# Optimization experiments

Measured on AMD Instinct MI355X. Metric: run time of the kernel, lower is better.

## Reference

```python
import jax, jax.numpy as jnp
import numpy as np

NUM_GRAPHS = 1024


def setup_inputs() -> dict:
    key = jax.random.key(0)
    k1, k2, k3, k4 = jax.random.split(key, 4)
    N, IN, OUT = 500000, 128, 128
    x = jax.random.normal(k1, (N, IN), dtype=jnp.float32)
    batch_id = jnp.sort(jax.random.randint(k2, (N,), 0, NUM_GRAPHS))
    # torch Linear: weight [out_features, in_features_total]
    W = jax.random.normal(k3, (OUT, 2 * IN), dtype=jnp.float32) * (1.0 / np.sqrt(2 * IN))
    b = jax.random.normal(k4, (OUT,), dtype=jnp.float32) * 0.01
    return {"x": x, "batch_id": batch_id, "W": W, "b": b}


def reference(x, batch_id, W, b):
    # global_mean_pool: segment-mean of x over batch_id -> [G, IN]
    sums = jax.ops.segment_sum(x, batch_id, num_segments=NUM_GRAPHS)
    counts = jax.ops.segment_sum(jnp.ones((x.shape[0],), dtype=x.dtype), batch_id,
                                 num_segments=NUM_GRAPHS)
    mean = sums / jnp.maximum(counts, 1.0)[:, None]  # [G, IN]
    # gather per-graph context back to each node, concat, linear
    g_per_node = mean[batch_id]                      # [N, IN]
    inp = jnp.concatenate([x, g_per_node], axis=-1)  # [N, 2*IN]
    return inp @ W.T + b                             # [N, OUT]
```

## Files before the change

kernel.cpp:

```cpp
#include <hip/hip_runtime.h>
#include <hip/hip_bf16.h>


#define G_NUM 1024
#define IN_F 128
#define OUT_F 128

typedef __attribute__((ext_vector_type(8))) short short8;
typedef __attribute__((ext_vector_type(4))) float f32x4;

static __device__ __forceinline__ unsigned short f2bf(float f) {
    union { float f; unsigned u; } v; v.f = f;
    unsigned u = v.u;
    unsigned r = (u + 0x7FFFu + ((u >> 16) & 1u)) >> 16;
    return (unsigned short)r;
}

static __device__ __forceinline__ short8 pack8(float4 a, float4 b) {
    short8 o;
    o[0] = (short)f2bf(a.x); o[1] = (short)f2bf(a.y);
    o[2] = (short)f2bf(a.z); o[3] = (short)f2bf(a.w);
    o[4] = (short)f2bf(b.x); o[5] = (short)f2bf(b.y);
    o[6] = (short)f2bf(b.z); o[7] = (short)f2bf(b.w);
    return o;
}

__global__ void k_wcvt(const float* __restrict__ W, unsigned short* __restrict__ W1b) {
    int i = blockIdx.x * 256 + threadIdx.x;
    if (i < OUT_F * IN_F) {
        int o = i >> 7, k = i & 127;
        W1b[i] = f2bf(W[o * 256 + k]);
    }
}

__global__ __launch_bounds__(256) void k_mean_ctx(
        const float* __restrict__ x, const int* __restrict__ bid,
        const float* __restrict__ W, const float* __restrict__ b,
        float* __restrict__ ctx, int N) {
    int g = blockIdx.x;
    int tid = threadIdx.x;

    int lo = 0, hi = N;
    while (lo < hi) { int m = (lo + hi) >> 1; if (bid[m] < g) lo = m + 1; else hi = m; }
    int start = lo;
    int lo2 = start, hi2 = N;
    while (lo2 < hi2) { int m = (lo2 + hi2) >> 1; if (bid[m] < g + 1) lo2 = m + 1; else hi2 = m; }
    int end = lo2;
    int cnt = end - start;

    __shared__ float4 red[8][32];
    __shared__ float ms[IN_F];

    int c4 = tid & 31;
    int rg = tid >> 5;
    float4 s0 = make_float4(0.f, 0.f, 0.f, 0.f);
    float4 s1 = s0, s2 = s0, s3 = s0;

    int r = start + rg;
    for (; r + 24 < end; r += 32) {
        float4 a = *(const float4*)(x + (size_t)(r     ) * IN_F + c4 * 4);
        float4 c = *(const float4*)(x + (size_t)(r +  8) * IN_F + c4 * 4);
        float4 d = *(const float4*)(x + (size_t)(r + 16) * IN_F + c4 * 4);
        float4 e = *(const float4*)(x + (size_t)(r + 24) * IN_F + c4 * 4);
        s0.x += a.x; s0.y += a.y; s0.z += a.z; s0.w += a.w;
        s1.x += c.x; s1.y += c.y; s1.z += c.z; s1.w += c.w;
        s2.x += d.x; s2.y += d.y; s2.z += d.z; s2.w += d.w;
        s3.x += e.x; s3.y += e.y; s3.z += e.z; s3.w += e.w;
    }
    for (; r < end; r += 8) {
        float4 a = *(const float4*)(x + (size_t)r * IN_F + c4 * 4);
        s0.x += a.x; s0.y += a.y; s0.z += a.z; s0.w += a.w;
    }
    s0.x += s1.x + s2.x + s3.x;
    s0.y += s1.y + s2.y + s3.y;
    s0.z += s1.z + s2.z + s3.z;
    s0.w += s1.w + s2.w + s3.w;

    red[rg][c4] = s0;
    __syncthreads();
    if (tid < 32) {
        float4 t = red[0][tid];
        #pragma unroll
        for (int i = 1; i < 8; ++i) {
            float4 v = red[i][tid];
            t.x += v.x; t.y += v.y; t.z += v.z; t.w += v.w;
        }
        float inv = 1.0f / (float)(cnt > 0 ? cnt : 1);
        ms[tid * 4 + 0] = t.x * inv;
        ms[tid * 4 + 1] = t.y * inv;
        ms[tid * 4 + 2] = t.z * inv;
        ms[tid * 4 + 3] = t.w * inv;
    }
    __syncthreads();
    if (tid < OUT_F) {
        int o = tid;
        float acc = b[o];
        const float* w2 = W + o * 256 + 128;
        #pragma unroll 8
        for (int k = 0; k < IN_F; ++k) acc += ms[k] * w2[k];
        ctx[g * OUT_F + o] = acc;
    }
}

__global__ __launch_bounds__(256, 2) void k_gemm(
        const float* __restrict__ x, const int* __restrict__ bid,
        const unsigned short* __restrict__ W1b, const float* __restrict__ ctx,
        float* __restrict__ out, int N) {
    int tid = threadIdx.x;
    int row0 = blockIdx.x * 128;
    int lane = tid & 63, wave = tid >> 6;
    int l16 = lane & 15, quad = lane >> 4;
    int wrow = (wave & 1) * 64;
    int wcol = (wave >> 1) * 64;

    f32x4 acc[4][4];
    #pragma unroll
    for (int mt = 0; mt < 4; ++mt)
        #pragma unroll
        for (int ot = 0; ot < 4; ++ot)
            acc[mt][ot] = (f32x4){0.f, 0.f, 0.f, 0.f};

    #pragma unroll
    for (int kt = 0; kt < 4; ++kt) {
        short8 bf[4];
        #pragma unroll
        for (int ot = 0; ot < 4; ++ot)
            bf[ot] = *(const short8*)(W1b + (wcol + ot * 16 + l16) * IN_F + kt * 32 + quad * 8);
        short8 af[4];
        #pragma unroll
        for (int mt = 0; mt < 4; ++mt) {
            int r = row0 + wrow + mt * 16 + l16;
            float4 v0 = make_float4(0.f, 0.f, 0.f, 0.f), v1 = v0;
            if (r < N) {
                const float* p = x + (size_t)r * IN_F + kt * 32 + quad * 8;
                v0 = *(const float4*)p;
                v1 = *(const float4*)(p + 4);
            }
            af[mt] = pack8(v0, v1);
        }
        #pragma unroll
        for (int mt = 0; mt < 4; ++mt)
            #pragma unroll
            for (int ot = 0; ot < 4; ++ot)
                acc[mt][ot] = __builtin_amdgcn_mfma_f32_16x16x32_bf16(
                    af[mt], bf[ot], acc[mt][ot], 0, 0, 0);
    }

    int lastrow = row0 + 127 < N ? row0 + 127 : N - 1;
    int b_lo = bid[row0], b_hi = bid[lastrow];
    if (b_lo == b_hi) {
        float cv[4];
        #pragma unroll
        for (int ot = 0; ot < 4; ++ot)
            cv[ot] = ctx[b_lo * OUT_F + wcol + ot * 16 + l16];
        #pragma unroll
        for (int mt = 0; mt < 4; ++mt) {
            #pragma unroll
            for (int r4 = 0; r4 < 4; ++r4) {
                int row = row0 + wrow + mt * 16 + quad * 4 + r4;
                if (row < N) {
                    #pragma unroll
                    for (int ot = 0; ot < 4; ++ot)
                        out[(size_t)row * OUT_F + wcol + ot * 16 + l16] =
                            acc[mt][ot][r4] + cv[ot];
                }
            }
        }
    } else {
        #pragma unroll
        for (int mt = 0; mt < 4; ++mt) {
            #pragma unroll
            for (int r4 = 0; r4 < 4; ++r4) {
                int row = row0 + wrow + mt * 16 + quad * 4 + r4;
                if (row < N) {
                    int cb = bid[row] * OUT_F;
                    #pragma unroll
                    for (int ot = 0; ot < 4; ++ot)
                        out[(size_t)row * OUT_F + wcol + ot * 16 + l16] =
                            acc[mt][ot][r4] + ctx[cb + wcol + ot * 16 + l16];
                }
            }
        }
    }
}

extern "C" void kernel_launch(void* const* d_in, const int* in_sizes, int n_in,
                              void* d_out, int out_size, void* d_ws, size_t ws_size,
                              hipStream_t stream) {
    const float* x  = (const float*)d_in[0];
    const int* bid  = (const int*)d_in[1];
    const float* W  = (const float*)d_in[2];
    const float* b  = (const float*)d_in[3];
    float* out      = (float*)d_out;
    int N = in_sizes[1];

    float* ctx = (float*)d_ws;
    unsigned short* W1b = (unsigned short*)((char*)d_ws + (size_t)G_NUM * OUT_F * sizeof(float));

    k_wcvt<<<(OUT_F * IN_F + 255) / 256, 256, 0, stream>>>(W, W1b);
    k_mean_ctx<<<G_NUM, 256, 0, stream>>>(x, bid, W, b, ctx, N);
    k_gemm<<<(N + 127) / 128, 256, 0, stream>>>(x, bid, W1b, ctx, out, N);
}
```

Baseline: 548.5 us.

## Write bf16 copy of x during pooling pass and feed GEMM from it

The pooling kernel now also converts x to bf16 and stores it in workspace, and folds the weight conversion in, removing one launch. A new GEMM reads the half-size bf16 copy instead of fp32 x, uses a 32x128 per-wave tile and allows 3 blocks per SM. The bf16 write adds about 128MB of traffic in pass 1, in exchange for reading 128MB instead of 256MB in the GEMM. There is a fallback to the old path when the workspace is too small.

```diff
diff --git a/kernel.cpp b/kernel.cpp
--- a/kernel.cpp
+++ b/kernel.cpp
@@ -1,5 +1,4 @@
 #include <hip/hip_runtime.h>
-#include <hip/hip_bf16.h>
 
 
 #define G_NUM 1024
@@ -8,12 +7,18 @@
 
 typedef __attribute__((ext_vector_type(8))) short short8;
 typedef __attribute__((ext_vector_type(4))) float f32x4;
+typedef __attribute__((ext_vector_type(4))) unsigned short us4;
 
 static __device__ __forceinline__ unsigned short f2bf(float f) {
     union { float f; unsigned u; } v; v.f = f;
     unsigned u = v.u;
-    unsigned r = (u + 0x7FFFu + ((u >> 16) & 1u)) >> 16;
-    return (unsigned short)r;
+    return (unsigned short)((u + 0x7FFFu + ((u >> 16) & 1u)) >> 16);
+}
+
+static __device__ __forceinline__ us4 pack4(float4 a) {
+    us4 o;
+    o[0] = f2bf(a.x); o[1] = f2bf(a.y); o[2] = f2bf(a.z); o[3] = f2bf(a.w);
+    return o;
 }
 
 static __device__ __forceinline__ short8 pack8(float4 a, float4 b) {
@@ -25,20 +30,19 @@
     return o;
 }
 
-__global__ void k_wcvt(const float* __restrict__ W, unsigned short* __restrict__ W1b) {
-    int i = blockIdx.x * 256 + threadIdx.x;
-    if (i < OUT_F * IN_F) {
-        int o = i >> 7, k = i & 127;
-        W1b[i] = f2bf(W[o * 256 + k]);
-    }
-}
-
-__global__ __launch_bounds__(256) void k_mean_ctx(
+template <bool WXB>
+__global__ __launch_bounds__(256) void k_pass1(
         const float* __restrict__ x, const int* __restrict__ bid,
         const float* __restrict__ W, const float* __restrict__ b,
-        float* __restrict__ ctx, int N) {
+        float* __restrict__ ctx, unsigned short* __restrict__ W1b,
+        unsigned short* __restrict__ xb, int N) {
     int g = blockIdx.x;
     int tid = threadIdx.x;
+
+    if (tid < 16) {
+        int i = (g << 4) + tid;
+        W1b[i] = f2bf(W[(i >> 7) * 256 + (i & 127)]);
+    }
 
     int lo = 0, hi = N;
     while (lo < hi) { int m = (lo + hi) >> 1; if (bid[m] < g) lo = m + 1; else hi = m; }
@@ -62,6 +66,12 @@
         float4 c = *(const float4*)(x + (size_t)(r +  8) * IN_F + c4 * 4);
         float4 d = *(const float4*)(x + (size_t)(r + 16) * IN_F + c4 * 4);
         float4 e = *(const float4*)(x + (size_t)(r + 24) * IN_F + c4 * 4);
+        if (WXB) {
+            *(us4*)(xb + (size_t)(r     ) * IN_F + c4 * 4) = pack4(a);
+            *(us4*)(xb + (size_t)(r +  8) * IN_F + c4 * 4) = pack4(c);
+            *(us4*)(xb + (size_t)(r + 16) * IN_F + c4 * 4) = pack4(d);
+            *(us4*)(xb + (size_t)(r + 24) * IN_F + c4 * 4) = pack4(e);
+        }
         s0.x += a.x; s0.y += a.y; s0.z += a.z; s0.w += a.w;
         s1.x += c.x; s1.y += c.y; s1.z += c.z; s1.w += c.w;
         s2.x += d.x; s2.y += d.y; s2.z += d.z; s2.w += d.w;
@@ -69,6 +79,7 @@
     }
     for (; r < end; r += 8) {
         float4 a = *(const float4*)(x + (size_t)r * IN_F + c4 * 4);
+        if (WXB) *(us4*)(xb + (size_t)r * IN_F + c4 * 4) = pack4(a);
         s0.x += a.x; s0.y += a.y; s0.z += a.z; s0.w += a.w;
     }
     s0.x += s1.x + s2.x + s3.x;
@@ -102,7 +113,81 @@
     }
 }
 
-__global__ __launch_bounds__(256, 2) void k_gemm(
+__global__ __launch_bounds__(256, 3) void k_gemm_bf(
+        const unsigned short* __restrict__ xb, const int* __restrict__ bid,
+        const unsigned short* __restrict__ W1b, const float* __restrict__ ctx,
+        float* __restrict__ out, int N) {
+    int tid = threadIdx.x;
+    int row0 = blockIdx.x * 128;
+    int lane = tid & 63, wave = tid >> 6;
+    int l16 = lane & 15, quad = lane >> 4;
+    int wrow = wave * 32;
+
+    f32x4 acc[2][8];
+    #pragma unroll
+    for (int mt = 0; mt < 2; ++mt)
+        #pragma unroll
+        for (int ot = 0; ot < 8; ++ot)
+            acc[mt][ot] = (f32x4){0.f, 0.f, 0.f, 0.f};
+
+    #pragma unroll
+    for (int kt = 0; kt < 4; ++kt) {
+        short8 af[2];
+        #pragma unroll
+        for (int mt = 0; mt < 2; ++mt) {
+            int rrow = row0 + wrow + mt * 16 + l16;
+            short8 v = (short8){0, 0, 0, 0, 0, 0, 0, 0};
+            if (rrow < N)
+                v = *(const short8*)(xb + (size_t)rrow * IN_F + kt * 32 + quad * 8);
+            af[mt] = v;
+        }
+        #pragma unroll
+        for (int ot = 0; ot < 8; ++ot) {
+            short8 bf = *(const short8*)(W1b + (ot * 16 + l16) * IN_F + kt * 32 + quad * 8);
+            acc[0][ot] = __builtin_amdgcn_mfma_f32_16x16x32_bf16(af[0], bf, acc[0][ot], 0, 0, 0);
+            acc[1][ot] = __builtin_amdgcn_mfma_f32_16x16x32_bf16(af[1], bf, acc[1][ot], 0, 0, 0);
+        }
+    }
+
+    int lastrow = row0 + 127 < N ? row0 + 127 : N - 1;
+    int b_lo = bid[row0], b_hi = bid[lastrow];
+    if (b_lo == b_hi) {
+        float cv[8];
+        #pragma unroll
+        for (int ot = 0; ot < 8; ++ot)
+            cv[ot] = ctx[b_lo * OUT_F + ot * 16 + l16];
+        #pragma unroll
+        for (int mt = 0; mt < 2; ++mt) {
+            #pragma unroll
+            for (int r4 = 0; r4 < 4; ++r4) {
+                int row = row0 + wrow + mt * 16 + quad * 4 + r4;
+                if (row < N) {
+                    #pragma unroll
+                    for (int ot = 0; ot < 8; ++ot)
+                        out[(size_t)row * OUT_F + ot * 16 + l16] =
+                            acc[mt][ot][r4] + cv[ot];
+                }
+            }
+        }
+    } else {
+        #pragma unroll
+        for (int mt = 0; mt < 2; ++mt) {
+            #pragma unroll
+            for (int r4 = 0; r4 < 4; ++r4) {
+                int row = row0 + wrow + mt * 16 + quad * 4 + r4;
+                if (row < N) {
+                    int cb = bid[row] * OUT_F;
+                    #pragma unroll
+                    for (int ot = 0; ot < 8; ++ot)
+                        out[(size_t)row * OUT_F + ot * 16 + l16] =
+                            acc[mt][ot][r4] + ctx[cb + ot * 16 + l16];
+                }
+            }
+        }
+    }
+}
+
+__global__ __launch_bounds__(256, 2) void k_gemm_f32(
         const float* __restrict__ x, const int* __restrict__ bid,
         const unsigned short* __restrict__ W1b, const float* __restrict__ ctx,
         float* __restrict__ out, int N) {
@@ -194,10 +279,18 @@
     float* out      = (float*)d_out;
     int N = in_sizes[1];
 
+    size_t ctx_bytes = (size_t)G_NUM * OUT_F * sizeof(float);
+    size_t w1b_bytes = (size_t)OUT_F * IN_F * sizeof(unsigned short);
     float* ctx = (float*)d_ws;
-    unsigned short* W1b = (unsigned short*)((char*)d_ws + (size_t)G_NUM * OUT_F * sizeof(float));
-
-    k_wcvt<<<(OUT_F * IN_F + 255) / 256, 256, 0, stream>>>(W, W1b);
-    k_mean_ctx<<<G_NUM, 256, 0, stream>>>(x, bid, W, b, ctx, N);
-    k_gemm<<<(N + 127) / 128, 256, 0, stream>>>(x, bid, W1b, ctx, out, N);
-}
+    unsigned short* W1b = (unsigned short*)((char*)d_ws + ctx_bytes);
+    unsigned short* xb  = (unsigned short*)((char*)d_ws + ctx_bytes + w1b_bytes);
+    size_t need = ctx_bytes + w1b_bytes + (size_t)N * IN_F * sizeof(unsigned short);
+
+    if (ws_size >= need) {
+        k_pass1<true><<<G_NUM, 256, 0, stream>>>(x, bid, W, b, ctx, W1b, xb, N);
+        k_gemm_bf<<<(N + 127) / 128, 256, 0, stream>>>(xb, bid, W1b, ctx, out, N);
+    } else {
+        k_pass1<false><<<G_NUM, 256, 0, stream>>>(x, bid, W, b, ctx, W1b, nullptr, N);
+        k_gemm_f32<<<(N + 127) / 128, 256, 0, stream>>>(x, bid, W1b, ctx, out, N);
+    }
+}
```

Measured after the change: 541.0 us. Within noise of the previous version (-1.4%).
